# Kernel optimization log

Measured on AMD Instinct MI355X. Metric: run time of the kernel, lower is better.

Reference implementation:

```python
import jax, jax.numpy as jnp
import numpy as np

H = 16
D_MODEL = 2048
D_K = D_MODEL // H


def setup_inputs() -> dict:
    key = jax.random.key(0)
    ks = jax.random.split(key, 5)
    B, S = 4, 2048
    x = jax.random.normal(ks[0], (B, S, D_MODEL), dtype=jnp.float32)
    scale = 1.0 / np.sqrt(D_MODEL)
    Wq = jax.random.normal(ks[1], (D_MODEL, D_MODEL), dtype=jnp.float32) * scale
    Wk = jax.random.normal(ks[2], (D_MODEL, D_MODEL), dtype=jnp.float32) * scale
    Wv = jax.random.normal(ks[3], (D_MODEL, D_MODEL), dtype=jnp.float32) * scale
    Wo = jax.random.normal(ks[4], (D_MODEL, D_MODEL), dtype=jnp.float32) * scale
    return {"x": x, "Wq": Wq, "Wk": Wk, "Wv": Wv, "Wo": Wo, "use_mask": 1}


def reference(x, Wq, Wk, Wv, Wo, use_mask):
    B, S, _ = x.shape
    # nn.Linear with no bias: y = x @ W.T; then split heads -> [B, H, S, d_k]
    def proj(W):
        return (x @ W.T).reshape(B, S, H, D_K).transpose(0, 2, 1, 3)

    q, k, v = proj(Wq), proj(Wk), proj(Wv)
    scores = jnp.einsum("bhqd,bhkd->bhqk", q, k) / jnp.sqrt(jnp.float32(D_K))
    if use_mask:
        causal = jnp.tril(jnp.ones((S, S), dtype=bool))  # [S, S]
        scores = jnp.where(causal, scores, -jnp.inf)
    probs = jax.nn.softmax(scores, axis=-1)
    out = jnp.einsum("bhqk,bhkd->bhqd", probs, v)
    out = out.transpose(0, 2, 1, 3).reshape(B, S, H * D_K)
    return out @ Wo.T
```

## Files before the change

kernel.cpp:

```cpp
#include <hip/hip_runtime.h>
#include <hip/hip_bf16.h>

typedef __bf16 bf16_t;
typedef __bf16 bf16x8 __attribute__((ext_vector_type(8)));
typedef float f32x4 __attribute__((ext_vector_type(4)));

#define B_  4
#define S_  2048
#define H_  16
#define DK_ 128
#define DM_ 2048
#define BS_ (B_ * S_)

static __device__ __forceinline__ f32x4 mfma16(bf16x8 a, bf16x8 b, f32x4 c) {
  return __builtin_amdgcn_mfma_f32_16x16x32_bf16(a, b, c, 0, 0, 0);
}

static __device__ __forceinline__ void async_copy16(const bf16_t* g, bf16_t* l) {
  __builtin_amdgcn_global_load_lds(
      (const __attribute__((address_space(1))) void*)g,
      (__attribute__((address_space(3))) void*)l, 16, 0, 0);
}

#define BARRIER() asm volatile("s_barrier" ::: "memory")
#define WAIT_VM6() asm volatile("s_waitcnt vmcnt(6)" ::: "memory")

template <int CTRL>
static __device__ __forceinline__ float dpp_rorf(float x) {
  return __builtin_bit_cast(float,
      __builtin_amdgcn_update_dpp(0, __builtin_bit_cast(int, x), CTRL, 0xF, 0xF, true));
}
static __device__ __forceinline__ float rowmax16(float r) {
  r = fmaxf(r, dpp_rorf<0x121>(r));
  r = fmaxf(r, dpp_rorf<0x122>(r));
  r = fmaxf(r, dpp_rorf<0x124>(r));
  r = fmaxf(r, dpp_rorf<0x128>(r));
  return r;
}
static __device__ __forceinline__ float rowsum16(float r) {
  r += dpp_rorf<0x121>(r);
  r += dpp_rorf<0x122>(r);
  r += dpp_rorf<0x124>(r);
  r += dpp_rorf<0x128>(r);
  return r;
}

struct ChainOn  { static constexpr bool v = true;  };
struct ChainOff { static constexpr bool v = false; };

__global__ __launch_bounds__(256) void cvt_bf16(const float* __restrict__ in,
                                                bf16_t* __restrict__ out, int n8) {
  int i = blockIdx.x * 256 + threadIdx.x;
  if (i < n8) {
    const float4* p = (const float4*)in + (size_t)i * 2;
    float4 f0 = p[0], f1 = p[1];
    bf16x8 r;
    r[0] = (bf16_t)f0.x; r[1] = (bf16_t)f0.y; r[2] = (bf16_t)f0.z; r[3] = (bf16_t)f0.w;
    r[4] = (bf16_t)f1.x; r[5] = (bf16_t)f1.y; r[6] = (bf16_t)f1.z; r[7] = (bf16_t)f1.w;
    ((bf16x8*)out)[i] = r;
  }
}

template <typename TC>
static __device__ __forceinline__ void gemm_body(
    const bf16_t* __restrict__ A, const bf16_t* __restrict__ B, TC* __restrict__ C,
    bool vtout, int b256, bf16_t (&Ab)[2][2][8192], bf16_t (&Bb)[2][2][8192]) {
  const int tid  = threadIdx.x;
  const int wave = tid >> 6;
  const int lane = tid & 63;
  const int quad = lane >> 4;
  const int l16  = lane & 15;
  const int wm   = (wave >> 2) * 128;
  const int wn   = (wave & 3) * 64;

  const int xcd = b256 & 7;
  const int idx = b256 >> 3;
  const int bm  = (xcd * 4 + (idx >> 3)) * 256;
  const int bn  = (idx & 7) * 256;
  const int K   = DM_;

  const int r0 = wave * 16 + (lane >> 2);
  const int r1 = r0 + 128;
  const int s0 = (r0 + (r0 >> 2)) & 3;
  const int s1 = (r1 + (r1 >> 2)) & 3;
  const size_t aO0 = (size_t)(bm + r0) * K + ((lane & 3) ^ s0) * 8;
  const size_t aO1 = (size_t)(bm + r1) * K + ((lane & 3) ^ s1) * 8;
  const size_t bO0 = (size_t)(bn + r0) * K + ((lane & 3) ^ s0) * 8;
  const size_t bO1 = (size_t)(bn + r1) * K + ((lane & 3) ^ s1) * 8;
  const int dst0 = wave * 512;
  const int dst1 = 4096 + wave * 512;

  auto stA = [&](int buf, int kh, int kt) __attribute__((always_inline)) {
    const size_t c = (size_t)kt * 64 + kh * 32;
    async_copy16(A + aO0 + c, &Ab[buf][kh][dst0]);
    async_copy16(A + aO1 + c, &Ab[buf][kh][dst1]);
  };
  auto stB = [&](int buf, int kh, int kt) __attribute__((always_inline)) {
    const size_t c = (size_t)kt * 64 + kh * 32;
    async_copy16(B + bO0 + c, &Bb[buf][kh][dst0]);
    async_copy16(B + bO1 + c, &Bb[buf][kh][dst1]);
  };

  const int sw = (l16 + (l16 >> 2)) & 3;
  const int qs = (quad ^ sw) * 8;

  f32x4 acc[8][4];
#pragma unroll
  for (int i = 0; i < 8; ++i)
#pragma unroll
    for (int j = 0; j < 4; ++j) acc[i][j] = (f32x4){0.f, 0.f, 0.f, 0.f};

  bf16x8 af[4], bfr[4];

  auto lda = [&](int buf, int kh, int mh) __attribute__((always_inline)) {
#pragma unroll
    for (int i = 0; i < 4; ++i)
      af[i] = *(const bf16x8*)(&Ab[buf][kh][(wm + mh * 64 + i * 16 + l16) * 32 + qs]);
  };
  auto ldb = [&](int buf, int kh) __attribute__((always_inline)) {
#pragma unroll
    for (int n = 0; n < 4; ++n)
      bfr[n] = *(const bf16x8*)(&Bb[buf][kh][(wn + n * 16 + l16) * 32 + qs]);
  };
  auto mma = [&](int mh) __attribute__((always_inline)) {
    __builtin_amdgcn_s_setprio(1);
#pragma unroll
    for (int i = 0; i < 4; ++i)
#pragma unroll
      for (int n = 0; n < 4; ++n)
        acc[mh * 4 + i][n] = mfma16(af[i], bfr[n], acc[mh * 4 + i][n]);
    __builtin_amdgcn_s_setprio(0);
  };

  const int NT    = K >> 6;
  const int ITERS = NT >> 1;

  stB(0, 0, 0); stA(0, 0, 0); stB(0, 1, 0); stA(0, 1, 0);
  stB(1, 0, 1); stA(1, 0, 1); stB(1, 1, 1);
  WAIT_VM6();
  BARRIER();

  for (int I = 0; I < ITERS; ++I) {
    const int o   = 2 * I + 1;
    const int te2 = (2 * I + 2 < NT) ? 2 * I + 2 : NT - 1;
    const int to2 = (2 * I + 3 < NT) ? 2 * I + 3 : NT - 1;

    lda(0, 0, 0); ldb(0, 0);
    stA(1, 1, o);
    BARRIER();
    mma(0);
    BARRIER();
    lda(0, 0, 1);
    stB(0, 0, te2);
    BARRIER();
    mma(1);
    BARRIER();
    lda(0, 1, 0); ldb(0, 1);
    stA(0, 0, te2);
    BARRIER();
    mma(0);
    BARRIER();
    lda(0, 1, 1);
    stB(0, 1, te2);
    BARRIER();
    mma(1);
    WAIT_VM6();
    BARRIER();
    lda(1, 0, 0); ldb(1, 0);
    stA(0, 1, te2);
    BARRIER();
    mma(0);
    BARRIER();
    lda(1, 0, 1);
    stB(1, 0, to2);
    BARRIER();
    mma(1);
    BARRIER();
    lda(1, 1, 0); ldb(1, 1);
    stA(1, 0, to2);
    BARRIER();
    mma(0);
    BARRIER();
    lda(1, 1, 1);
    stB(1, 1, to2);
    BARRIER();
    mma(1);
    WAIT_VM6();
    BARRIER();
  }

  asm volatile("s_waitcnt vmcnt(0)" ::: "memory");

#pragma unroll
  for (int mt = 0; mt < 8; ++mt)
#pragma unroll
    for (int nt = 0; nt < 4; ++nt)
#pragma unroll
      for (int v = 0; v < 4; ++v) {
        int row = bm + wm + mt * 16 + quad * 4 + v;
        int col = bn + wn + nt * 16 + l16;
        if (vtout) {
          size_t o = (size_t)(((row >> 11) * 16 + (col >> 7)) * 128 + (col & 127)) * S_ +
                     (row & 2047);
          C[o] = (TC)acc[mt][nt][v];
        } else {
          C[(size_t)row * DM_ + col] = (TC)acc[mt][nt][v];
        }
      }
}

__global__ __launch_bounds__(512, 2) void qkv_gemm(
    const bf16_t* __restrict__ xb, const bf16_t* __restrict__ wq,
    const bf16_t* __restrict__ wk, const bf16_t* __restrict__ wv,
    bf16_t* __restrict__ Qb, bf16_t* __restrict__ Kb, bf16_t* __restrict__ Vt) {
  __shared__ bf16_t Ab[2][2][8192];
  __shared__ bf16_t Bb[2][2][8192];
  const int seg  = (int)blockIdx.x >> 8;
  const int b256 = (int)blockIdx.x & 255;
  const bf16_t* W = (seg == 0) ? wq : (seg == 1) ? wk : wv;
  bf16_t* C       = (seg == 0) ? Qb : (seg == 1) ? Kb : Vt;
  gemm_body<bf16_t>(xb, W, C, seg == 2, b256, Ab, Bb);
}

__global__ __launch_bounds__(512, 2) void out_gemm(
    const bf16_t* __restrict__ Ob, const bf16_t* __restrict__ Wob,
    float* __restrict__ out) {
  __shared__ bf16_t Ab[2][2][8192];
  __shared__ bf16_t Bb[2][2][8192];
  gemm_body<float>(Ob, Wob, out, false, (int)blockIdx.x, Ab, Bb);
}

__global__ __launch_bounds__(256, 2) void attn_kernel(const bf16_t* __restrict__ Q,
                                                      const bf16_t* __restrict__ K,
                                                      const bf16_t* __restrict__ VT,
                                                      bf16_t* __restrict__ O,
                                                      const int* __restrict__ use_mask) {
  __shared__ bf16_t Ks[2 * 64 * 128];
  __shared__ bf16_t Vs[2 * 128 * 64];
  __shared__ bf16_t Ps[2 * 4 * 16 * 64];

  const int tid  = threadIdx.x;
  const int wave = tid >> 6;
  const int lane = tid & 63;
  const int quad = lane >> 4;
  const int l16  = lane & 15;

  const int lid  = (int)(blockIdx.y * gridDim.x + blockIdx.x);
  const int xcd  = lid & 7;
  const int t8   = lid >> 3;
  const int bh   = xcd + ((t8 >> 4) << 3);
  const int pair = t8 & 15;
  const int qa   = 31 - pair;
  const int qc   = pair;
  const int b = bh >> 4, h = bh & 15;
  const int maskflag = *use_mask;

  const size_t qbaseA = ((size_t)b * S_ + (size_t)qa * 64) * DM_ + h * DK_;
  const size_t qbaseC = ((size_t)b * S_ + (size_t)qc * 64) * DM_ + h * DK_;

  int skO[4], svO[4];
#pragma unroll
  for (int p = 0; p < 4; ++p) {
    int rK = p * 16 + wave * 4 + quad;
    skO[p] = rK * DM_ + ((l16 ^ (rK & 7)) * 8);
    int dV = p * 32 + wave * 8 + (lane >> 3);
    svO[p] = dV * S_ + (((lane & 7) ^ (dV & 7)) * 8);
  }

  const bf16_t* Kbase = K + (size_t)b * S_ * DM_ + h * DK_;
  const bf16_t* Vbase = VT + (size_t)bh * DK_ * S_;

  auto stage_kv = [&](int j, int buf) __attribute__((always_inline)) {
    const bf16_t* kb = Kbase + (size_t)j * 64 * DM_;
    const bf16_t* vb = Vbase + (size_t)j * 64;
    bf16_t* kl = Ks + buf * 8192 + wave * 512;
    bf16_t* vl = Vs + buf * 8192 + wave * 512;
#pragma unroll
    for (int p = 0; p < 4; ++p) {
      async_copy16(kb + skO[p], kl + p * 2048);
      async_copy16(vb + svO[p], vl + p * 2048);
    }
  };

  bf16x8 qfA[4], qfC[4];
#pragma unroll
  for (int kk = 0; kk < 4; ++kk) {
    size_t ro = (size_t)(wave * 16 + l16) * DM_ + kk * 32 + quad * 8;
    qfA[kk] = *(const bf16x8*)(Q + qbaseA + ro);
    qfC[kk] = *(const bf16x8*)(Q + qbaseC + ro);
  }

  stage_kv(0, 0);

  f32x4 accA[8], accC[8];
#pragma unroll
  for (int i = 0; i < 8; ++i) {
    accA[i] = (f32x4){0.f, 0.f, 0.f, 0.f};
    accC[i] = (f32x4){0.f, 0.f, 0.f, 0.f};
  }
  float mA[4], lA[4], mC[4], lC[4];
#pragma unroll
  for (int v = 0; v < 4; ++v) {
    mA[v] = -INFINITY; lA[v] = 0.f;
    mC[v] = -INFINITY; lC[v] = 0.f;
  }

  bf16_t* PwA = Ps + wave * 1024;
  bf16_t* PwC = Ps + 4096 + wave * 1024;

  const float c1 = 0.08838834764831845f * 1.4426950408889634f;

  const int ntA = maskflag ? qa + 1 : (S_ / 64);
  const int ntC = maskflag ? qc + 1 : (S_ / 64);

  auto softmax_chain = [&](f32x4 (&s)[4], float (&mrow)[4], float (&lrow)[4],
                           f32x4 (&acc)[8], bf16_t* Pw, bool masked)
      __attribute__((always_inline)) {
#pragma unroll
    for (int v = 0; v < 4; ++v) {
      float x[4];
#pragma unroll
      for (int nt = 0; nt < 4; ++nt) {
        float y = s[nt][v] * c1;
        if (masked) {
          int kg = nt * 16 + l16;
          int qg = wave * 16 + quad * 4 + v;
          if (kg > qg) y = -INFINITY;
        }
        x[nt] = y;
      }
      float r = fmaxf(fmaxf(x[0], x[1]), fmaxf(x[2], x[3]));
      r = rowmax16(r);
      float m = mrow[v];
      if (r > m + 8.f) {
        float alpha = __builtin_amdgcn_exp2f(m - r);
        lrow[v] *= alpha;
#pragma unroll
        for (int dt = 0; dt < 8; ++dt) acc[dt][v] *= alpha;
        mrow[v] = r;
        m = r;
      }
      float rs = 0.f;
      int prow = quad * 4 + v;
#pragma unroll
      for (int nt = 0; nt < 4; ++nt) {
        float p = __builtin_amdgcn_exp2f(x[nt] - m);
        rs += p;
        Pw[prow * 64 + ((nt * 16 + l16) ^ ((prow & 7) << 3))] = (bf16_t)p;
      }
      lrow[v] += rowsum16(rs);
    }
  };

  auto body = [&](auto DOC, int cur, bool maskedA, bool maskedC)
      __attribute__((always_inline)) {
    constexpr bool doC = decltype(DOC)::v;
    const bf16_t* KsB = Ks + cur * 8192;
    const bf16_t* VsB = Vs + cur * 8192;

    f32x4 sA[4], sC[4];
#pragma unroll
    for (int nt = 0; nt < 4; ++nt) {
      sA[nt] = (f32x4){0.f, 0.f, 0.f, 0.f};
      sC[nt] = (f32x4){0.f, 0.f, 0.f, 0.f};
    }
    __builtin_amdgcn_s_setprio(1);
#pragma unroll
    for (int kk = 0; kk < 4; ++kk) {
#pragma unroll
      for (int nt = 0; nt < 4; ++nt) {
        bf16x8 kf = *(const bf16x8*)(KsB + (nt * 16 + l16) * 128 +
                                     ((kk * 32 + quad * 8) ^ ((l16 & 7) << 3)));
        sA[nt] = mfma16(qfA[kk], kf, sA[nt]);
        if constexpr (doC) sC[nt] = mfma16(qfC[kk], kf, sC[nt]);
      }
    }
    __builtin_amdgcn_s_setprio(0);

    softmax_chain(sA, mA, lA, accA, PwA, maskedA);
    if constexpr (doC) softmax_chain(sC, mC, lC, accC, PwC, maskedC);

    __builtin_amdgcn_s_setprio(1);
#pragma unroll
    for (int kk = 0; kk < 2; ++kk) {
      bf16x8 pfA = *(const bf16x8*)(PwA + l16 * 64 +
                                    ((kk * 32 + quad * 8) ^ ((l16 & 7) << 3)));
      bf16x8 pfC = {};
      if constexpr (doC)
        pfC = *(const bf16x8*)(PwC + l16 * 64 +
                               ((kk * 32 + quad * 8) ^ ((l16 & 7) << 3)));
#pragma unroll
      for (int dt = 0; dt < 8; ++dt) {
        bf16x8 vf = *(const bf16x8*)(VsB + (dt * 16 + l16) * 64 +
                                     ((kk * 32 + quad * 8) ^ ((l16 & 7) << 3)));
        accA[dt] = mfma16(pfA, vf, accA[dt]);
        if constexpr (doC) accC[dt] = mfma16(pfC, vf, accC[dt]);
      }
    }
    __builtin_amdgcn_s_setprio(0);
  };

  __syncthreads();

  for (int t = 0; t < ntA; ++t) {
    const int cur = t & 1;
    if (t + 1 < ntA) stage_kv(t + 1, cur ^ 1);
    const bool mAf = maskflag && (t == qa);
    if (t < ntC)
      body(ChainOn{},  cur, mAf, maskflag && (t == qc));
    else
      body(ChainOff{}, cur, mAf, false);
    __syncthreads();
  }

  auto epilogue = [&](f32x4 (&acc)[8], float (&lrow)[4], size_t qbase)
      __attribute__((always_inline)) {
    float rl[4];
#pragma unroll
    for (int v = 0; v < 4; ++v) rl[v] = __builtin_amdgcn_rcpf(lrow[v]);
#pragma unroll
    for (int dt = 0; dt < 8; ++dt)
#pragma unroll
      for (int v = 0; v < 4; ++v) {
        int qr = wave * 16 + quad * 4 + v;
        O[qbase + (size_t)qr * DM_ + dt * 16 + l16] = (bf16_t)(acc[dt][v] * rl[v]);
      }
  };
  epilogue(accA, lA, qbaseA);
  epilogue(accC, lC, qbaseC);
}

extern "C" void kernel_launch(void* const* d_in, const int* in_sizes, int n_in,
                              void* d_out, int out_size, void* d_ws, size_t ws_size,
                              hipStream_t stream) {
  const float* x  = (const float*)d_in[0];
  const float* Wq = (const float*)d_in[1];
  const float* Wk = (const float*)d_in[2];
  const float* Wv = (const float*)d_in[3];
  const float* Wo = (const float*)d_in[4];
  const int* use_mask = (const int*)d_in[5];
  float* out = (float*)d_out;

  const size_t TSZ = (size_t)BS_ * DM_;
  const size_t WSZ = (size_t)DM_ * DM_;
  bf16_t* Qb  = (bf16_t*)d_ws;
  bf16_t* Kb  = Qb + TSZ;
  bf16_t* Vt  = Kb + TSZ;
  bf16_t* xb  = Vt + TSZ;
  bf16_t* Ob  = xb;
  bf16_t* Wob = Vt;
  bf16_t* wq = (bf16_t*)d_out;
  bf16_t* wk = wq + WSZ;
  bf16_t* wv = wk + WSZ;

  cvt_bf16<<<(int)(TSZ / 8 / 256), 256, 0, stream>>>(x,  xb, (int)(TSZ / 8));
  cvt_bf16<<<(int)(WSZ / 8 / 256), 256, 0, stream>>>(Wq, wq, (int)(WSZ / 8));
  cvt_bf16<<<(int)(WSZ / 8 / 256), 256, 0, stream>>>(Wk, wk, (int)(WSZ / 8));
  cvt_bf16<<<(int)(WSZ / 8 / 256), 256, 0, stream>>>(Wv, wv, (int)(WSZ / 8));

  qkv_gemm<<<dim3(768), 512, 0, stream>>>(xb, wq, wk, wv, Qb, Kb, Vt);

  dim3 gA(16, 64);
  attn_kernel<<<gA, 256, 0, stream>>>(Qb, Kb, Vt, Ob, use_mask);

  cvt_bf16<<<(int)(WSZ / 8 / 256), 256, 0, stream>>>(Wo, Wob, (int)(WSZ / 8));
  out_gemm<<<dim3(256), 512, 0, stream>>>(Ob, Wob, out);
}
```

Baseline: 576.3 us.

## Restructure GEMM LDS layout to full 64-wide K tiles split by M/N halves

Changes the shared-memory staging in the projection GEMM so each buffer holds 128 rows by 64 K-values, with the split going along M/N halves instead of K halves. A new XOR swizzle is applied to global-to-LDS copies and to fragment reads. The main loop now works on quadrant sub-tiles with two K steps per MFMA group, and waits at vmcnt(2) instead of vmcnt(6). The goal is fewer LDS bank conflicts and better fragment reuse, at the cost of a tighter prefetch window and a riskier schedule.

Measured after the change: 584.3 us. Within noise of the previous version (+1.4%).

```diff
diff --git a/kernel.cpp b/kernel.cpp
--- a/kernel.cpp
+++ b/kernel.cpp
@@ -23,7 +23,7 @@
 }
 
 #define BARRIER() asm volatile("s_barrier" ::: "memory")
-#define WAIT_VM6() asm volatile("s_waitcnt vmcnt(6)" ::: "memory")
+#define WAIT_VM2() asm volatile("s_waitcnt vmcnt(2)" ::: "memory")
 
 template <int CTRL>
 static __device__ __forceinline__ float dpp_rorf(float x) {
@@ -70,8 +70,11 @@
   const int lane = tid & 63;
   const int quad = lane >> 4;
   const int l16  = lane & 15;
-  const int wm   = (wave >> 2) * 128;
-  const int wn   = (wave & 3) * 64;
+  const int wm    = (wave >> 2) * 128;
+  const int wn    = (wave & 3) * 64;
+  const int mhalf = wave >> 2;
+  const int nhalf = (wave & 3) >> 1;
+  const int nrow0 = (wave & 1) * 64;
 
   const int xcd = b256 & 7;
   const int idx = b256 >> 3;
@@ -79,30 +82,29 @@
   const int bn  = (idx & 7) * 256;
   const int K   = DM_;
 
-  const int r0 = wave * 16 + (lane >> 2);
-  const int r1 = r0 + 128;
-  const int s0 = (r0 + (r0 >> 2)) & 3;
-  const int s1 = (r1 + (r1 >> 2)) & 3;
-  const size_t aO0 = (size_t)(bm + r0) * K + ((lane & 3) ^ s0) * 8;
-  const size_t aO1 = (size_t)(bm + r1) * K + ((lane & 3) ^ s1) * 8;
-  const size_t bO0 = (size_t)(bn + r0) * K + ((lane & 3) ^ s0) * 8;
-  const size_t bO1 = (size_t)(bn + r1) * K + ((lane & 3) ^ s1) * 8;
-  const int dst0 = wave * 512;
-  const int dst1 = 4096 + wave * 512;
-
-  auto stA = [&](int buf, int kh, int kt) __attribute__((always_inline)) {
-    const size_t c = (size_t)kt * 64 + kh * 32;
-    async_copy16(A + aO0 + c, &Ab[buf][kh][dst0]);
-    async_copy16(A + aO1 + c, &Ab[buf][kh][dst1]);
-  };
-  auto stB = [&](int buf, int kh, int kt) __attribute__((always_inline)) {
-    const size_t c = (size_t)kt * 64 + kh * 32;
-    async_copy16(B + bO0 + c, &Bb[buf][kh][dst0]);
-    async_copy16(B + bO1 + c, &Bb[buf][kh][dst1]);
-  };
-
-  const int sw = (l16 + (l16 >> 2)) & 3;
-  const int qs = (quad ^ sw) * 8;
+  const bf16_t* Ablk = A + (size_t)bm * (size_t)K;
+  const bf16_t* Bblk = B + (size_t)bn * (size_t)K;
+
+  int srcO[2];
+#pragma unroll
+  for (int i = 0; i < 2; ++i) {
+    int g = i * 512 + wave * 64 + lane;
+    int row = g >> 3, gc = g & 7;
+    srcO[i] = row * K + ((gc ^ (((row >> 2) & 1) << 1)) * 8);
+  }
+  const int dstO0 = wave * 512;
+  const int dstO1 = 4096 + wave * 512;
+
+  auto stgA = [&](int buf, int half, int kt) __attribute__((always_inline)) {
+    const bf16_t* src = Ablk + (size_t)(half * 128) * K + kt * 64;
+    async_copy16(src + srcO[0], &Ab[buf][half][dstO0]);
+    async_copy16(src + srcO[1], &Ab[buf][half][dstO1]);
+  };
+  auto stgB = [&](int buf, int half, int kt) __attribute__((always_inline)) {
+    const bf16_t* src = Bblk + (size_t)(half * 128) * K + kt * 64;
+    async_copy16(src + srcO[0], &Bb[buf][half][dstO0]);
+    async_copy16(src + srcO[1], &Bb[buf][half][dstO1]);
+  };
 
   f32x4 acc[8][4];
 #pragma unroll
@@ -110,82 +112,95 @@
 #pragma unroll
     for (int j = 0; j < 4; ++j) acc[i][j] = (f32x4){0.f, 0.f, 0.f, 0.f};
 
-  bf16x8 af[4], bfr[4];
-
-  auto lda = [&](int buf, int kh, int mh) __attribute__((always_inline)) {
-#pragma unroll
-    for (int i = 0; i < 4; ++i)
-      af[i] = *(const bf16x8*)(&Ab[buf][kh][(wm + mh * 64 + i * 16 + l16) * 32 + qs]);
-  };
-  auto ldb = [&](int buf, int kh) __attribute__((always_inline)) {
-#pragma unroll
-    for (int n = 0; n < 4; ++n)
-      bfr[n] = *(const bf16x8*)(&Bb[buf][kh][(wn + n * 16 + l16) * 32 + qs]);
-  };
-  auto mma = [&](int mh) __attribute__((always_inline)) {
+  bf16x8 af[8], bf0[4], bf1[4];
+
+  auto rdA = [&](int buf, int mq) __attribute__((always_inline)) {
+#pragma unroll
+    for (int mf = 0; mf < 4; ++mf) {
+      int row = mq * 64 + mf * 16 + l16;
+      int sw  = ((row >> 2) & 1) << 4;
+#pragma unroll
+      for (int kk = 0; kk < 2; ++kk)
+        af[mf * 2 + kk] =
+            *(const bf16x8*)(&Ab[buf][mhalf][(row * 64 + kk * 32 + quad * 8) ^ sw]);
+    }
+  };
+  auto rdB = [&](bf16x8 (&dst)[4], int buf, int nq) __attribute__((always_inline)) {
+#pragma unroll
+    for (int nf = 0; nf < 2; ++nf) {
+      int row = nrow0 + nq * 32 + nf * 16 + l16;
+      int sw  = ((row >> 2) & 1) << 4;
+#pragma unroll
+      for (int kk = 0; kk < 2; ++kk)
+        dst[nf * 2 + kk] =
+            *(const bf16x8*)(&Bb[buf][nhalf][(row * 64 + kk * 32 + quad * 8) ^ sw]);
+    }
+  };
+  auto mmaq = [&](int mq, int nq, bf16x8 (&bq)[4]) __attribute__((always_inline)) {
     __builtin_amdgcn_s_setprio(1);
 #pragma unroll
-    for (int i = 0; i < 4; ++i)
-#pragma unroll
-      for (int n = 0; n < 4; ++n)
-        acc[mh * 4 + i][n] = mfma16(af[i], bfr[n], acc[mh * 4 + i][n]);
+    for (int mf = 0; mf < 4; ++mf)
+#pragma unroll
+      for (int nf = 0; nf < 2; ++nf)
+#pragma unroll
+        for (int kk = 0; kk < 2; ++kk)
+          acc[mq * 4 + mf][nq * 2 + nf] =
+              mfma16(af[mf * 2 + kk], bq[nf * 2 + kk], acc[mq * 4 + mf][nq * 2 + nf]);
     __builtin_amdgcn_s_setprio(0);
   };
 
   const int NT    = K >> 6;
   const int ITERS = NT >> 1;
 
-  stB(0, 0, 0); stA(0, 0, 0); stB(0, 1, 0); stA(0, 1, 0);
-  stB(1, 0, 1); stA(1, 0, 1); stB(1, 1, 1);
-  WAIT_VM6();
+  stgA(0, 0, 0); stgA(0, 1, 0); stgB(0, 0, 0); stgB(0, 1, 0);
+  stgA(1, 0, 1);
+  WAIT_VM2();
   BARRIER();
 
   for (int I = 0; I < ITERS; ++I) {
-    const int o   = 2 * I + 1;
-    const int te2 = (2 * I + 2 < NT) ? 2 * I + 2 : NT - 1;
-    const int to2 = (2 * I + 3 < NT) ? 2 * I + 3 : NT - 1;
-
-    lda(0, 0, 0); ldb(0, 0);
-    stA(1, 1, o);
-    BARRIER();
-    mma(0);
-    BARRIER();
-    lda(0, 0, 1);
-    stB(0, 0, te2);
-    BARRIER();
-    mma(1);
-    BARRIER();
-    lda(0, 1, 0); ldb(0, 1);
-    stA(0, 0, te2);
-    BARRIER();
-    mma(0);
-    BARRIER();
-    lda(0, 1, 1);
-    stB(0, 1, te2);
-    BARRIER();
-    mma(1);
-    WAIT_VM6();
-    BARRIER();
-    lda(1, 0, 0); ldb(1, 0);
-    stA(0, 1, te2);
-    BARRIER();
-    mma(0);
-    BARRIER();
-    lda(1, 0, 1);
-    stB(1, 0, to2);
-    BARRIER();
-    mma(1);
-    BARRIER();
-    lda(1, 1, 0); ldb(1, 1);
-    stA(1, 0, to2);
-    BARRIER();
-    mma(0);
-    BARRIER();
-    lda(1, 1, 1);
-    stB(1, 1, to2);
-    BARRIER();
-    mma(1);
-    WAIT_VM6();
+    const int o  = 2 * I + 1;
+    const int e2 = (2 * I + 2 < NT) ? 2 * I + 2 : NT - 1;
+    const int o2 = (2 * I + 3 < NT) ? 2 * I + 3 : NT - 1;
+
+    rdA(0, 0); rdB(bf0, 0, 0);
+    stgA(1, 1, o);
+    BARRIER();
+    mmaq(0, 0, bf0);
+    BARRIER();
+    rdB(bf1, 0, 1);
+    stgB(1, 0, o);
+    BARRIER();
+    mmaq(0, 1, bf1);
+    BARRIER();
+    rdA(0, 1);
+    stgB(1, 1, o);
+    BARRIER();
+    mmaq(1, 0, bf0);
+    BARRIER();
+    stgA(0, 0, e2);
+    BARRIER();
+    mmaq(1, 1, bf1);
+    WAIT_VM2();
+    BARRIER();
+    rdA(1, 0); rdB(bf0, 1, 0);
+    stgA(0, 1, e2);
+    BARRIER();
+    mmaq(0, 0, bf0);
+    BARRIER();
+    rdB(bf1, 1, 1);
+    stgB(0, 0, e2);
+    BARRIER();
+    mmaq(0, 1, bf1);
+    BARRIER();
+    rdA(1, 1);
+    stgB(0, 1, e2);
+    BARRIER();
+    mmaq(1, 0, bf0);
+    BARRIER();
+    stgA(1, 0, o2);
+    BARRIER();
+    mmaq(1, 1, bf1);
+    WAIT_VM2();
     BARRIER();
   }
 
```
